# Performance work log

Measured on AMD Instinct MI355X. Metric: run time of the kernel, lower is better.

Reference implementation:

```python
import jax, jax.numpy as jnp
import numpy as np

TOP_K = 2


def setup_inputs() -> dict:
    key = jax.random.key(0)
    k1, k2, k3, k4, k5 = jax.random.split(key, 5)
    B, S, D, E, F = 2, 1024, 2048, 8, 768
    scale_in = 1.0 / np.sqrt(D)
    scale_ff = 1.0 / np.sqrt(F)
    return {
        "x": jax.random.normal(k1, (B, S, D), dtype=jnp.float32),
        "w_gate_router": jax.random.normal(k2, (E, D), dtype=jnp.float32) * scale_in,
        "w_gate_proj": jax.random.normal(k3, (E, F, D), dtype=jnp.float32) * scale_in,
        "w_up_proj": jax.random.normal(k4, (E, F, D), dtype=jnp.float32) * scale_in,
        "w_down_proj": jax.random.normal(k5, (E, D, F), dtype=jnp.float32) * scale_ff,
    }


def moe_forward(x, w_gate_router, w_gate_proj, w_up_proj, w_down_proj):
    E = w_gate_router.shape[0]
    # Router: scores [B,S,E], top-k selection, softmax over the k selected scores.
    scores = jnp.einsum("bsd,ed->bse", x, w_gate_router)
    topk_scores, topk_idx = jax.lax.top_k(scores, TOP_K)          # [B,S,K]
    topk_probs = jax.nn.softmax(topk_scores, axis=-1)             # [B,S,K]
    # Dense combine weights: zero for unselected experts (== scatter of topk_probs).
    weights = jnp.sum(topk_probs[..., None] * jax.nn.one_hot(topk_idx, E, dtype=x.dtype), axis=-2)  # [B,S,E]
    # Per-expert SwiGLU computed densely over all tokens (same math as
    # gather/dispatch-per-expert followed by scatter-add combine).
    gate = jnp.einsum("bsd,efd->bsef", x, w_gate_proj)            # [B,S,E,F]
    up = jnp.einsum("bsd,efd->bsef", x, w_up_proj)
    hidden = jax.nn.silu(gate) * up                                # [B,S,E,F]
    # Weighted combine: sum_e weights[b,s,e] * (hidden @ w_down[e].T)
    out = jnp.einsum("bsef,edf,bse->bsd", hidden, w_down_proj, weights)
    return out


def reference(x, w_gate_router, w_gate_proj, w_up_proj, w_down_proj):
    return moe_forward(x, w_gate_router, w_gate_proj, w_up_proj, w_down_proj)
```

## Files before the change

### kernel.cpp

```cpp
#include <hip/hip_runtime.h>

#define T_TOK 2048
#define DIM   2048
#define NEXP  8
#define FF    768
#define NGRP  16

typedef unsigned short u16;
typedef unsigned int   u32;
typedef __bf16 bf16x8 __attribute__((ext_vector_type(8)));
typedef float  f32x4  __attribute__((ext_vector_type(4)));
typedef u16    u16x4  __attribute__((ext_vector_type(4)));
typedef u16    u16x8  __attribute__((ext_vector_type(8)));

#define AS1 __attribute__((address_space(1)))
#define AS3 __attribute__((address_space(3)))

__device__ __forceinline__ u16 f2bf(float f) {
    union { u32 i; float f; } v; v.f = f;
    u32 r = v.i + 0x7FFF + ((v.i >> 16) & 1);
    return (u16)(r >> 16);
}
__device__ __forceinline__ float bf2f(u16 u) {
    union { u32 i; float f; } v; v.i = ((u32)u) << 16; return v.f;
}

__device__ __forceinline__ void gload16(const u16* g, u16* l) {
    __builtin_amdgcn_global_load_lds((const AS1 u32*)g, (AS3 u32*)l, 16, 0, 0);
}

__global__ void cvt3_kernel(const float* __restrict__ s0, u16* __restrict__ d0,
                            const float* __restrict__ s1, u16* __restrict__ d1,
                            const float* __restrict__ s2, u16* __restrict__ d2, int n4) {
    const float* s; u16* d;
    switch (blockIdx.y) {
        case 0: s = s0; d = d0; break;
        case 1: s = s1; d = d1; break;
        default: s = s2; d = d2; break;
    }
    int i = blockIdx.x * blockDim.x + threadIdx.x;
    int st = gridDim.x * blockDim.x;
    for (; i < n4; i += st) {
        f32x4 v = ((const f32x4*)s)[i];
        u16x4 o;
#pragma unroll
        for (int j = 0; j < 4; j++) o[j] = f2bf(v[j]);
        ((u16x4*)d)[i] = o;
    }
}

__global__ void router_kernel(const float* __restrict__ x, const float* __restrict__ wr,
                              int* cnt, int* rt_e, float* rt_p, u16* __restrict__ xb) {
    int wave = threadIdx.x >> 6, lane = threadIdx.x & 63;
    int t = blockIdx.x * 4 + wave;
    float xv[32];
#pragma unroll
    for (int i = 0; i < 32; i++) xv[i] = x[(size_t)t * DIM + i * 64 + lane];
#pragma unroll
    for (int i = 0; i < 32; i++) xb[(size_t)t * DIM + i * 64 + lane] = f2bf(xv[i]);
    float s[NEXP];
#pragma unroll
    for (int e = 0; e < NEXP; e++) {
        float acc = 0.f;
#pragma unroll
        for (int i = 0; i < 32; i++) acc += xv[i] * wr[(size_t)e * DIM + i * 64 + lane];
        for (int off = 32; off; off >>= 1) acc += __shfl_xor(acc, off);
        s[e] = acc;
    }
    if (lane == 0) {
        int bi = 0; float bv = s[0];
        for (int e = 1; e < NEXP; e++) if (s[e] > bv) { bv = s[e]; bi = e; }
        float sv = -1e30f; int si = 0;
        for (int e = 0; e < NEXP; e++) { if (e == bi) continue; if (s[e] > sv) { sv = s[e]; si = e; } }
        float p0 = 1.f / (1.f + __expf(sv - bv));
        float p1 = 1.f - p0;
        rt_e[t * 2 + 0] = bi; rt_e[t * 2 + 1] = si;
        rt_p[t * 2 + 0] = p0; rt_p[t * 2 + 1] = p1;
        atomicAdd(&cnt[bi * 2 + 0], 1);
        atomicAdd(&cnt[si * 2 + 1], 1);
    }
}

__global__ void scan_kernel(const int* cnt, int* base, int* tile_g, int* tile_m0, int* ntiles) {
    int lane = threadIdx.x;
    int c = (lane < NGRP) ? cnt[lane] : 0;
    int nt_g = (c + 127) >> 7;
    int pre = 0, tpre = 0;
    for (int i = 0; i < NGRP; i++) {
        int ci = __shfl(c, i), ti = __shfl(nt_g, i);
        if (i < lane) { pre += ci; tpre += ti; }
    }
    if (lane < NGRP) {
        base[lane] = pre;
        for (int j = 0; j < nt_g; j++) { tile_g[tpre + j] = lane; tile_m0[tpre + j] = j * 128; }
        if (lane == NGRP - 1) *ntiles = tpre + nt_g;
    }
}

__global__ void assign_kernel(const int* rt_e, const float* rt_p, const int* base,
                              int* poscnt, int* rowtok, float* rowprob) {
    int t = blockIdx.x * blockDim.x + threadIdx.x;
    if (t >= T_TOK) return;
    for (int k = 0; k < 2; k++) {
        int g = rt_e[t * 2 + k] * 2 + k;
        int pos = atomicAdd(&poscnt[g], 1);
        int row = base[g] + pos;
        rowtok[row] = t;
        rowprob[row] = rt_p[t * 2 + k];
    }
}

__launch_bounds__(256)
__global__ void gateup_kernel(const u16* __restrict__ xb, const u16* __restrict__ wgb,
                              const u16* __restrict__ wub,
                              const int* cnt, const int* base, const int* tile_g,
                              const int* tile_m0, const int* ntiles,
                              const int* rowtok, const float* rowprob,
                              u16* __restrict__ hidden) {
    int tile = blockIdx.x;
    if (tile >= *ntiles) return;
    int g = tile_g[tile], m0 = tile_m0[tile];
    int e = g >> 1;
    int f0 = blockIdx.y * 32;
    int cg = cnt[g], bg_ = base[g];

    __shared__ u16 As[128 * 32];
    __shared__ u16 Bs[64 * 32];
    __shared__ int   tks[128];
    __shared__ float ps[128];

    int tid = threadIdx.x;
    if (tid < 128) {
        int valid = (m0 + tid) < cg;
        tks[tid] = valid ? rowtok[bg_ + m0 + tid] : 0;
        ps[tid]  = valid ? rowprob[bg_ + m0 + tid] : 0.f;
    }
    __syncthreads();

    int wave = tid >> 6, lane = tid & 63;
    int quad = lane >> 4, l16 = lane & 15;
    int wr = wave >> 1, wc = wave & 1;

    int r4   = lane >> 2;
    int koff = (lane & 3) * 8;
    const u16* ga0 = xb + (size_t)tks[wave * 32 + r4] * DIM + koff;
    const u16* ga1 = xb + (size_t)tks[wave * 32 + 16 + r4] * DIM + koff;
    u16* lA0 = &As[(wave * 32) * 32];
    u16* lA1 = &As[(wave * 32 + 16) * 32];
    const u16* bsrc = (wave & 1) ? wub : wgb;
    const u16* gb = bsrc + ((size_t)e * FF + f0 + (wave >> 1) * 16 + r4) * DIM + koff;
    u16* lB = &Bs[(wave * 16) * 32];

    f32x4 acc[4][2] = {};

    for (int kk = 0; kk < DIM; kk += 32) {
        gload16(ga0 + kk, lA0);
        gload16(ga1 + kk, lA1);
        gload16(gb + kk, lB);
        __syncthreads();
        bf16x8 a[4], b[2];
#pragma unroll
        for (int mi = 0; mi < 4; mi++)
            a[mi] = *(const bf16x8*)&As[(wr * 64 + mi * 16 + l16) * 32 + quad * 8];
#pragma unroll
        for (int ni = 0; ni < 2; ni++)
            b[ni] = *(const bf16x8*)&Bs[(wc * 32 + ni * 16 + l16) * 32 + quad * 8];
#pragma unroll
        for (int mi = 0; mi < 4; mi++)
#pragma unroll
            for (int ni = 0; ni < 2; ni++)
                acc[mi][ni] = __builtin_amdgcn_mfma_f32_16x16x32_bf16(a[mi], b[ni], acc[mi][ni], 0, 0, 0);
        __syncthreads();
    }

    int f = f0 + wc * 16 + l16;
#pragma unroll
    for (int mi = 0; mi < 4; mi++) {
#pragma unroll
        for (int r = 0; r < 4; r++) {
            int m = wr * 64 + mi * 16 + quad * 4 + r;
            if (m0 + m < cg) {
                float gv = acc[mi][0][r], uv = acc[mi][1][r];
                float h = (gv / (1.f + __expf(-gv))) * uv * ps[m];
                hidden[(size_t)(bg_ + m0 + m) * FF + f] = f2bf(h);
            }
        }
    }
}

__launch_bounds__(256)
__global__ void down_kernel(const u16* __restrict__ hid, const u16* __restrict__ wdb,
                            const int* cnt, const int* base, const int* tile_g,
                            const int* tile_m0, const int* ntiles, const int* rowtok,
                            u16* __restrict__ out0, u16* __restrict__ out1) {
    int tile = blockIdx.x;
    if (tile >= *ntiles) return;
    int g = tile_g[tile], m0 = tile_m0[tile];
    int e = g >> 1, slot = g & 1;
    int d0 = blockIdx.y * 64;
    int cg = cnt[g], bg_ = base[g];

    __shared__ u16 As[128 * 32];
    __shared__ u16 Bs[64 * 32];
    __shared__ int tks[128];

    int tid = threadIdx.x;
    if (tid < 128) tks[tid] = ((m0 + tid) < cg) ? rowtok[bg_ + m0 + tid] : 0;
    __syncthreads();

    int wave = tid >> 6, lane = tid & 63;
    int quad = lane >> 4, l16 = lane & 15;
    int wr = wave >> 1, wc = wave & 1;

    int r4   = lane >> 2;
    int koff = (lane & 3) * 8;
    const u16* ga0 = hid + (size_t)(bg_ + m0 + wave * 32 + r4) * FF + koff;
    const u16* ga1 = hid + (size_t)(bg_ + m0 + wave * 32 + 16 + r4) * FF + koff;
    u16* lA0 = &As[(wave * 32) * 32];
    u16* lA1 = &As[(wave * 32 + 16) * 32];
    const u16* gb = wdb + ((size_t)e * DIM + d0 + wave * 16 + r4) * FF + koff;
    u16* lB = &Bs[(wave * 16) * 32];

    f32x4 acc[4][2] = {};

    for (int kk = 0; kk < FF; kk += 32) {
        gload16(ga0 + kk, lA0);
        gload16(ga1 + kk, lA1);
        gload16(gb + kk, lB);
        __syncthreads();
        bf16x8 a[4], b[2];
#pragma unroll
        for (int mi = 0; mi < 4; mi++)
            a[mi] = *(const bf16x8*)&As[(wr * 64 + mi * 16 + l16) * 32 + quad * 8];
#pragma unroll
        for (int ni = 0; ni < 2; ni++)
            b[ni] = *(const bf16x8*)&Bs[(wc * 32 + ni * 16 + l16) * 32 + quad * 8];
#pragma unroll
        for (int mi = 0; mi < 4; mi++)
#pragma unroll
            for (int ni = 0; ni < 2; ni++)
                acc[mi][ni] = __builtin_amdgcn_mfma_f32_16x16x32_bf16(a[mi], b[ni], acc[mi][ni], 0, 0, 0);
        __syncthreads();
    }

    u16* outp = slot ? out1 : out0;
#pragma unroll
    for (int mi = 0; mi < 4; mi++) {
#pragma unroll
        for (int ni = 0; ni < 2; ni++) {
            int d = d0 + wc * 32 + ni * 16 + l16;
#pragma unroll
            for (int r = 0; r < 4; r++) {
                int m = wr * 64 + mi * 16 + quad * 4 + r;
                if (m0 + m < cg) {
                    outp[(size_t)tks[m] * DIM + d] = f2bf(acc[mi][ni][r]);
                }
            }
        }
    }
}

__global__ void combine_kernel(const u16* __restrict__ o0, const u16* __restrict__ o1,
                               float* __restrict__ out) {
    int i = blockIdx.x * blockDim.x + threadIdx.x;
    u16x8 a = *(const u16x8*)(o0 + (size_t)i * 8);
    u16x8 b = *(const u16x8*)(o1 + (size_t)i * 8);
    f32x4 r0, r1;
#pragma unroll
    for (int j = 0; j < 4; j++) {
        r0[j] = bf2f(a[j]) + bf2f(b[j]);
        r1[j] = bf2f(a[4 + j]) + bf2f(b[4 + j]);
    }
    *(f32x4*)(out + (size_t)i * 8) = r0;
    *(f32x4*)(out + (size_t)i * 8 + 4) = r1;
}

extern "C" void kernel_launch(void* const* d_in, const int* in_sizes, int n_in,
                              void* d_out, int out_size, void* d_ws, size_t ws_size,
                              hipStream_t stream) {
    const float* x  = (const float*)d_in[0];
    const float* wr = (const float*)d_in[1];
    const float* wg = (const float*)d_in[2];
    const float* wu = (const float*)d_in[3];
    const float* wd = (const float*)d_in[4];
    float* out = (float*)d_out;

    char* W = (char*)d_ws;
    int*   cnt     = (int*)(W + 0);
    int*   poscnt  = (int*)(W + 64);
    int*   base    = (int*)(W + 128);
    int*   ntiles  = (int*)(W + 192);
    int*   tile_g  = (int*)(W + 256);
    int*   tile_m0 = (int*)(W + 512);
    int*   rt_e    = (int*)(W + 1024);
    float* rt_p    = (float*)(W + 20480);
    int*   rowtok  = (int*)(W + 40960);
    float* rowprob = (float*)(W + 61440);
    u16*   hidden  = (u16*)(W + 81920);
    u16*   xb      = (u16*)(W + ((size_t)8  << 20));
    u16*   wgb     = (u16*)(W + ((size_t)17 << 20));
    u16*   wub     = (u16*)(W + ((size_t)43 << 20));
    u16*   wdb     = (u16*)(W + ((size_t)69 << 20));
    u16*   out0    = (u16*)(W + ((size_t)17 << 20));
    u16*   out1    = (u16*)(W + ((size_t)26 << 20));

    hipMemsetAsync(W, 0, 256, stream);

    const int NW = NEXP * FF * DIM / 4;
    cvt3_kernel<<<dim3(1536, 3), 256, 0, stream>>>(wg, wgb, wu, wub, wd, wdb, NW);

    router_kernel<<<T_TOK / 4, 256, 0, stream>>>(x, wr, cnt, rt_e, rt_p, xb);
    scan_kernel<<<1, 64, 0, stream>>>(cnt, base, tile_g, tile_m0, ntiles);
    assign_kernel<<<8, 256, 0, stream>>>(rt_e, rt_p, base, poscnt, rowtok, rowprob);

    gateup_kernel<<<dim3(48, 24), 256, 0, stream>>>(xb, wgb, wub, cnt, base, tile_g, tile_m0,
                                                    ntiles, rowtok, rowprob, hidden);
    down_kernel<<<dim3(48, 32), 256, 0, stream>>>(hidden, wdb, cnt, base, tile_g, tile_m0,
                                                  ntiles, rowtok, out0, out1);
    combine_kernel<<<T_TOK * DIM / (256 * 8), 256, 0, stream>>>(out0, out1, out);
}
```

Measured before the change: 384.6 us.

## Double-buffer LDS tiles with BK=64 and XOR swizzle in gate-up and down GEMMs

Both grouped GEMM kernels now use a K tile of 64 instead of 32, keep two LDS buffers so the next tile's global-to-LDS loads are issued while MFMAs run on the current one, and apply an XOR column swizzle to the LDS layout. The aim is to hide global load latency, halve the number of barriers per K step, and cut LDS bank conflicts. In exchange, LDS use per block grows fourfold (about 49 KB), which may lower occupancy, and correctness depends on the swizzle matching between the store and read sides.

```diff
diff --git a/kernel.cpp b/kernel.cpp
--- a/kernel.cpp
+++ b/kernel.cpp
@@ -5,6 +5,7 @@
 #define NEXP  8
 #define FF    768
 #define NGRP  16
+#define BK    64
 
 typedef unsigned short u16;
 typedef unsigned int   u32;
@@ -124,8 +125,8 @@
     int f0 = blockIdx.y * 32;
     int cg = cnt[g], bg_ = base[g];
 
-    __shared__ u16 As[128 * 32];
-    __shared__ u16 Bs[64 * 32];
+    __shared__ u16 As[2][128 * BK];
+    __shared__ u16 Bs[2][64 * BK];
     __shared__ int   tks[128];
     __shared__ float ps[128];
 
@@ -141,35 +142,62 @@
     int quad = lane >> 4, l16 = lane & 15;
     int wr = wave >> 1, wc = wave & 1;
 
-    int r4   = lane >> 2;
-    int koff = (lane & 3) * 8;
-    const u16* ga0 = xb + (size_t)tks[wave * 32 + r4] * DIM + koff;
-    const u16* ga1 = xb + (size_t)tks[wave * 32 + 16 + r4] * DIM + koff;
-    u16* lA0 = &As[(wave * 32) * 32];
-    u16* lA1 = &As[(wave * 32 + 16) * 32];
+    int r8  = lane >> 3;
+    int csw = ((lane & 7) ^ r8) * 8;
+
+    const u16* gA[4]; int lA[4];
+#pragma unroll
+    for (int gi = 0; gi < 4; gi++) {
+        int row = wave * 32 + gi * 8 + r8;
+        gA[gi] = xb + (size_t)tks[row] * DIM + csw;
+        lA[gi] = (wave * 32 + gi * 8) * BK;
+    }
     const u16* bsrc = (wave & 1) ? wub : wgb;
-    const u16* gb = bsrc + ((size_t)e * FF + f0 + (wave >> 1) * 16 + r4) * DIM + koff;
-    u16* lB = &Bs[(wave * 16) * 32];
+    const u16* gB[2]; int lB[2];
+#pragma unroll
+    for (int gi = 0; gi < 2; gi++) {
+        int f = f0 + (wave >> 1) * 16 + gi * 8 + r8;
+        gB[gi] = bsrc + ((size_t)e * FF + f) * DIM + csw;
+        lB[gi] = (wave * 16 + gi * 8) * BK;
+    }
 
     f32x4 acc[4][2] = {};
 
-    for (int kk = 0; kk < DIM; kk += 32) {
-        gload16(ga0 + kk, lA0);
-        gload16(ga1 + kk, lA1);
-        gload16(gb + kk, lB);
-        __syncthreads();
-        bf16x8 a[4], b[2];
-#pragma unroll
-        for (int mi = 0; mi < 4; mi++)
-            a[mi] = *(const bf16x8*)&As[(wr * 64 + mi * 16 + l16) * 32 + quad * 8];
-#pragma unroll
-        for (int ni = 0; ni < 2; ni++)
-            b[ni] = *(const bf16x8*)&Bs[(wc * 32 + ni * 16 + l16) * 32 + quad * 8];
-#pragma unroll
-        for (int mi = 0; mi < 4; mi++)
+#pragma unroll
+    for (int gi = 0; gi < 4; gi++) gload16(gA[gi], &As[0][0] + lA[gi]);
+#pragma unroll
+    for (int gi = 0; gi < 2; gi++) gload16(gB[gi], &Bs[0][0] + lB[gi]);
+    __syncthreads();
+
+    int sw0 = ((0 * 4 + quad) ^ (l16 & 7)) * 8;
+    int sw1 = ((1 * 4 + quad) ^ (l16 & 7)) * 8;
+
+#pragma unroll 2
+    for (int kt = 0; kt < DIM / BK; kt++) {
+        int cur = kt & 1;
+        int kk = (kt + 1) * BK;
+        if (kk < DIM) {
+#pragma unroll
+            for (int gi = 0; gi < 4; gi++) gload16(gA[gi] + kk, &As[cur ^ 1][0] + lA[gi]);
+#pragma unroll
+            for (int gi = 0; gi < 2; gi++) gload16(gB[gi] + kk, &Bs[cur ^ 1][0] + lB[gi]);
+        }
+#pragma unroll
+        for (int ks = 0; ks < 2; ks++) {
+            int sw = ks ? sw1 : sw0;
+            bf16x8 a[4], b[2];
+#pragma unroll
+            for (int mi = 0; mi < 4; mi++)
+                a[mi] = *(const bf16x8*)&As[cur][(wr * 64 + mi * 16 + l16) * BK + sw];
 #pragma unroll
             for (int ni = 0; ni < 2; ni++)
-                acc[mi][ni] = __builtin_amdgcn_mfma_f32_16x16x32_bf16(a[mi], b[ni], acc[mi][ni], 0, 0, 0);
+                b[ni] = *(const bf16x8*)&Bs[cur][(wc * 32 + ni * 16 + l16) * BK + sw];
+#pragma unroll
+            for (int mi = 0; mi < 4; mi++)
+#pragma unroll
+                for (int ni = 0; ni < 2; ni++)
+                    acc[mi][ni] = __builtin_amdgcn_mfma_f32_16x16x32_bf16(a[mi], b[ni], acc[mi][ni], 0, 0, 0);
+        }
         __syncthreads();
     }
 
@@ -200,8 +228,8 @@
     int d0 = blockIdx.y * 64;
     int cg = cnt[g], bg_ = base[g];
 
-    __shared__ u16 As[128 * 32];
-    __shared__ u16 Bs[64 * 32];
+    __shared__ u16 As[2][128 * BK];
+    __shared__ u16 Bs[2][64 * BK];
     __shared__ int tks[128];
 
     int tid = threadIdx.x;
@@ -212,34 +240,61 @@
     int quad = lane >> 4, l16 = lane & 15;
     int wr = wave >> 1, wc = wave & 1;
 
-    int r4   = lane >> 2;
-    int koff = (lane & 3) * 8;
-    const u16* ga0 = hid + (size_t)(bg_ + m0 + wave * 32 + r4) * FF + koff;
-    const u16* ga1 = hid + (size_t)(bg_ + m0 + wave * 32 + 16 + r4) * FF + koff;
-    u16* lA0 = &As[(wave * 32) * 32];
-    u16* lA1 = &As[(wave * 32 + 16) * 32];
-    const u16* gb = wdb + ((size_t)e * DIM + d0 + wave * 16 + r4) * FF + koff;
-    u16* lB = &Bs[(wave * 16) * 32];
+    int r8  = lane >> 3;
+    int csw = ((lane & 7) ^ r8) * 8;
+
+    const u16* gA[4]; int lA[4];
+#pragma unroll
+    for (int gi = 0; gi < 4; gi++) {
+        int row = wave * 32 + gi * 8 + r8;
+        gA[gi] = hid + (size_t)(bg_ + m0 + row) * FF + csw;
+        lA[gi] = (wave * 32 + gi * 8) * BK;
+    }
+    const u16* gB[2]; int lB[2];
+#pragma unroll
+    for (int gi = 0; gi < 2; gi++) {
+        int n = wave * 16 + gi * 8 + r8;
+        gB[gi] = wdb + ((size_t)e * DIM + d0 + n) * FF + csw;
+        lB[gi] = (wave * 16 + gi * 8) * BK;
+    }
 
     f32x4 acc[4][2] = {};
 
-    for (int kk = 0; kk < FF; kk += 32) {
-        gload16(ga0 + kk, lA0);
-        gload16(ga1 + kk, lA1);
-        gload16(gb + kk, lB);
-        __syncthreads();
-        bf16x8 a[4], b[2];
-#pragma unroll
-        for (int mi = 0; mi < 4; mi++)
-            a[mi] = *(const bf16x8*)&As[(wr * 64 + mi * 16 + l16) * 32 + quad * 8];
-#pragma unroll
-        for (int ni = 0; ni < 2; ni++)
-            b[ni] = *(const bf16x8*)&Bs[(wc * 32 + ni * 16 + l16) * 32 + quad * 8];
-#pragma unroll
-        for (int mi = 0; mi < 4; mi++)
+#pragma unroll
+    for (int gi = 0; gi < 4; gi++) gload16(gA[gi], &As[0][0] + lA[gi]);
+#pragma unroll
+    for (int gi = 0; gi < 2; gi++) gload16(gB[gi], &Bs[0][0] + lB[gi]);
+    __syncthreads();
+
+    int sw0 = ((0 * 4 + quad) ^ (l16 & 7)) * 8;
+    int sw1 = ((1 * 4 + quad) ^ (l16 & 7)) * 8;
+
+#pragma unroll 2
+    for (int kt = 0; kt < FF / BK; kt++) {
+        int cur = kt & 1;
+        int kk = (kt + 1) * BK;
+        if (kk < FF) {
+#pragma unroll
+            for (int gi = 0; gi < 4; gi++) gload16(gA[gi] + kk, &As[cur ^ 1][0] + lA[gi]);
+#pragma unroll
+            for (int gi = 0; gi < 2; gi++) gload16(gB[gi] + kk, &Bs[cur ^ 1][0] + lB[gi]);
+        }
+#pragma unroll
+        for (int ks = 0; ks < 2; ks++) {
+            int sw = ks ? sw1 : sw0;
+            bf16x8 a[4], b[2];
+#pragma unroll
+            for (int mi = 0; mi < 4; mi++)
+                a[mi] = *(const bf16x8*)&As[cur][(wr * 64 + mi * 16 + l16) * BK + sw];
 #pragma unroll
             for (int ni = 0; ni < 2; ni++)
-                acc[mi][ni] = __builtin_amdgcn_mfma_f32_16x16x32_bf16(a[mi], b[ni], acc[mi][ni], 0, 0, 0);
+                b[ni] = *(const bf16x8*)&Bs[cur][(wc * 32 + ni * 16 + l16) * BK + sw];
+#pragma unroll
+            for (int mi = 0; mi < 4; mi++)
+#pragma unroll
+                for (int ni = 0; ni < 2; ni++)
+                    acc[mi][ni] = __builtin_amdgcn_mfma_f32_16x16x32_bf16(a[mi], b[ni], acc[mi][ni], 0, 0, 0);
+        }
         __syncthreads();
     }
 
```

New measurement: 369.7 us. 3.9% less time.
